# Optimization experiments

Hardware: AMD Instinct MI355X
Metric: run time of the kernel (lower is better)

Reference implementation:

```python
import jax, jax.numpy as jnp
import numpy as np

E, D, H, K, N = 8, 512, 2048, 2, 1024  # experts, d_model, d_hidden, top_k, tokens
EPS = 1e-5


def _moe_linear(x, idx, W, b):
    # x: (M, in); idx: (M,) expert id per row; W: (E, out, in); b: (E, out)
    # Brute-force: compute per-expert dense GEMMs, select via one-hot (matches
    # BruteForceMoELinear math: y[i] = x[i] @ W[idx[i]].T + b[idx[i]]).
    m = jax.nn.one_hot(idx, W.shape[0], dtype=x.dtype)  # (M, E)
    y = jnp.einsum('me,eoi,mi->mo', m, W, x)
    return y + jnp.take(b, idx, axis=0)


def _forward(inp, gate_w, gate_b, w1, b1, w2, b2, ln_w, ln_b):
    # NaiveGate: linear -> top_k -> softmax over top-k logits
    logits = inp @ gate_w.T + gate_b              # (N, E)
    top_val, top_idx = jax.lax.top_k(logits, K)   # (N, K)
    score = jax.nn.softmax(top_val, axis=-1)      # (N, K)
    # repeat_interleave tokens, dispatch to experts
    x = jnp.repeat(inp, K, axis=0)                # (N*K, D)
    idx = top_idx.reshape(-1)                     # (N*K,)
    x = _moe_linear(x, idx, w1, b1)               # (N*K, H)
    x = jax.nn.gelu(x, approximate=False)         # torch F.gelu default = erf
    x = _moe_linear(x, idx, w2, b2)               # (N*K, D)
    x = x.reshape(N, K, D)
    x = jnp.einsum('nk,nkd->nd', score, x)        # bmm((N,1,K),(N,K,D)) combine
    # post layer norm (pre_lnorm=False)
    mu = jnp.mean(x, axis=-1, keepdims=True)
    var = jnp.var(x, axis=-1, keepdims=True)
    return (x - mu) * jax.lax.rsqrt(var + EPS) * ln_w + ln_b


def setup_inputs() -> dict:
    key = jax.random.key(0)
    ks = jax.random.split(key, 8)
    s = 0.02
    return {
        'inp': jax.random.normal(ks[0], (N, D), dtype=jnp.float32),
        'gate_w': s * jax.random.normal(ks[1], (E, D), dtype=jnp.float32),
        'gate_b': jnp.zeros((E,), dtype=jnp.float32),
        'w1': s * jax.random.normal(ks[2], (E, H, D), dtype=jnp.float32),
        'b1': jnp.zeros((E, H), dtype=jnp.float32),
        'w2': s * jax.random.normal(ks[3], (E, D, H), dtype=jnp.float32),
        'b2': jnp.zeros((E, D), dtype=jnp.float32),
        'ln_w': jnp.ones((D,), dtype=jnp.float32),
        'ln_b': jnp.zeros((D,), dtype=jnp.float32),
    }


def reference(inp, gate_w, gate_b, w1, b1, w2, b2, ln_w, ln_b):
    return _forward(inp, gate_w, gate_b, w1, b1, w2, b2, ln_w, ln_b)
```

## Files before the change

### kernel.cpp

```cpp
#include <hip/hip_runtime.h>
#include <cstdint>
#include <cstddef>

typedef _Float16 half_t;
typedef _Float16 half8 __attribute__((ext_vector_type(8)));
typedef float floatx4 __attribute__((ext_vector_type(4)));

#define E_ 8
#define D_ 512
#define H_ 2048
#define NTOK 1024
#define NP 2048
#define TM 64
#define MAX_TILES 40

__device__ __forceinline__ float gelu_f(float x) {
    return 0.5f * x * (1.0f + erff(x * 0.7071067811865476f));
}

__device__ __forceinline__ half8 cvt8(floatx4 a, floatx4 b) {
    half8 h = { (half_t)a[0], (half_t)a[1], (half_t)a[2], (half_t)a[3],
                (half_t)b[0], (half_t)b[1], (half_t)b[2], (half_t)b[3] };
    return h;
}

__global__ __launch_bounds__(256) void gate_kernel(
        const float* __restrict__ inp, const float* __restrict__ gate_w,
        const float* __restrict__ gate_b, float* __restrict__ logits) {
    int n = blockIdx.x * 4 + (threadIdx.x >> 6);
    int lane = threadIdx.x & 63;
    const floatx4* xr = (const floatx4*)(inp + (size_t)n * D_);
    floatx4 x0 = xr[lane * 2], x1 = xr[lane * 2 + 1];
    #pragma unroll
    for (int e = 0; e < E_; e++) {
        const floatx4* gr = (const floatx4*)(gate_w + (size_t)e * D_);
        floatx4 g0 = gr[lane * 2], g1 = gr[lane * 2 + 1];
        float p = x0[0]*g0[0] + x0[1]*g0[1] + x0[2]*g0[2] + x0[3]*g0[3]
                + x1[0]*g1[0] + x1[1]*g1[1] + x1[2]*g1[2] + x1[3]*g1[3];
        #pragma unroll
        for (int m = 1; m < 64; m <<= 1) p += __shfl_xor(p, m);
        if (lane == 0) logits[(size_t)n * E_ + e] = p + gate_b[e];
    }
}

__global__ __launch_bounds__(256) void plan_kernel(
        const float* __restrict__ logits, float* __restrict__ score,
        int* __restrict__ idx, int* __restrict__ pos_of_pair,
        int* __restrict__ tok_of_pos,
        int* __restrict__ tile_e, int* __restrict__ tile_row0,
        int* __restrict__ tile_cnt, int* __restrict__ ntiles) {
    __shared__ int cnt_s[E_], off_s[E_ + 1], cur_s[E_];
    int tid = threadIdx.x;
    if (tid < E_) { cnt_s[tid] = 0; cur_s[tid] = 0; }
    __syncthreads();
    int my_e[4][2];
    #pragma unroll
    for (int i = 0; i < 4; i++) {
        int n = tid + i * 256;
        float l[E_];
        #pragma unroll
        for (int e = 0; e < E_; e++) l[e] = logits[(size_t)n * E_ + e];
        int e0 = 0; float v0 = l[0];
        #pragma unroll
        for (int e = 1; e < E_; e++) if (l[e] > v0) { v0 = l[e]; e0 = e; }
        int e1 = -1; float v1 = -3.4e38f;
        #pragma unroll
        for (int e = 0; e < E_; e++) if (e != e0 && l[e] > v1) { v1 = l[e]; e1 = e; }
        float s1 = expf(v1 - v0);
        float den = 1.0f + s1;
        score[2 * n]     = 1.0f / den;
        score[2 * n + 1] = s1 / den;
        idx[2 * n]     = e0;
        idx[2 * n + 1] = e1;
        atomicAdd(&cnt_s[e0], 1);
        atomicAdd(&cnt_s[e1], 1);
        my_e[i][0] = e0; my_e[i][1] = e1;
    }
    __syncthreads();
    if (tid == 0) {
        int o = 0;
        #pragma unroll
        for (int e = 0; e < E_; e++) { off_s[e] = o; o += cnt_s[e]; }
        off_s[E_] = o;
        int t = 0;
        for (int e = 0; e < E_; e++) {
            int c = cnt_s[e];
            int nt = (c + TM - 1) / TM;
            for (int i = 0; i < nt; i++) {
                tile_e[t] = e;
                tile_row0[t] = off_s[e] + i * TM;
                int rem = c - i * TM;
                tile_cnt[t] = rem < TM ? rem : TM;
                t++;
            }
        }
        ntiles[0] = t;
    }
    __syncthreads();
    #pragma unroll
    for (int i = 0; i < 4; i++) {
        #pragma unroll
        for (int k = 0; k < 2; k++) {
            int p = (tid + i * 256) * 2 + k;
            int e = my_e[i][k];
            int r = atomicAdd(&cur_s[e], 1);
            int pos = off_s[e] + r;
            pos_of_pair[p] = pos;
            tok_of_pos[pos] = p >> 1;
        }
    }
}

__global__ __launch_bounds__(256) void gemm1_kernel(
        const float* __restrict__ inp, const int* __restrict__ tok_of_pos,
        const float* __restrict__ w1, const float* __restrict__ b1,
        const int* __restrict__ tile_e, const int* __restrict__ tile_row0,
        const int* __restrict__ tile_cnt, const int* __restrict__ ntiles,
        half_t* __restrict__ Y1) {
    __shared__ half_t As[2][64 * 64];
    __shared__ half_t Bs[2][64 * 64];
    int flat = blockIdx.x + gridDim.x * blockIdx.y;
    int per = (gridDim.x * gridDim.y) >> 3;
    int f2 = (flat & 7) * per + (flat >> 3);
    int t = f2 % MAX_TILES;
    int cb = f2 / MAX_TILES;
    if (t >= ntiles[0]) return;
    int e = tile_e[t], row0 = tile_row0[t], cnt = tile_cnt[t];
    int colbase = cb * 64;
    int tid = threadIdx.x;
    int wave = tid >> 6, lane = tid & 63;
    int quad = lane >> 4, l16 = lane & 15;
    int wm = (wave & 1) * 32, wn = (wave >> 1) * 32;
    int xm = l16 & 7;

    int gr0 = tid >> 3, gr1 = gr0 + 32, gc = tid & 7;
    int sw0 = gc ^ (gr0 & 7), sw1 = gc ^ (gr1 & 7);
    int ar0 = row0 + gr0; if (ar0 > NP - 1) ar0 = NP - 1;
    int ar1 = row0 + gr1; if (ar1 > NP - 1) ar1 = NP - 1;
    int tok0 = tok_of_pos[ar0];
    int tok1 = tok_of_pos[ar1];
    const floatx4* Ag0 = (const floatx4*)(inp + (size_t)tok0 * D_) + gc * 2;
    const floatx4* Ag1 = (const floatx4*)(inp + (size_t)tok1 * D_) + gc * 2;
    const floatx4* Bg0 = (const floatx4*)(w1 + ((size_t)e * H_ + colbase + gr0) * D_) + gc * 2;
    const floatx4* Bg1 = (const floatx4*)(w1 + ((size_t)e * H_ + colbase + gr1) * D_) + gc * 2;
    int sa0 = gr0 * 64 + sw0 * 8, sa1 = gr1 * 64 + sw1 * 8;

    floatx4 ra0a, ra0b, ra1a, ra1b, rb0a, rb0b, rb1a, rb1b;
    #define LOAD1(kq) do { \
        ra0a = Ag0[kq]; ra0b = Ag0[(kq) + 1]; \
        ra1a = Ag1[kq]; ra1b = Ag1[(kq) + 1]; \
        rb0a = Bg0[kq]; rb0b = Bg0[(kq) + 1]; \
        rb1a = Bg1[kq]; rb1b = Bg1[(kq) + 1]; } while (0)
    #define CVW1(buf) do { \
        *(half8*)(&As[buf][sa0]) = cvt8(ra0a, ra0b); \
        *(half8*)(&As[buf][sa1]) = cvt8(ra1a, ra1b); \
        *(half8*)(&Bs[buf][sa0]) = cvt8(rb0a, rb0b); \
        *(half8*)(&Bs[buf][sa1]) = cvt8(rb1a, rb1b); } while (0)

    floatx4 acc[2][2] = {};
    LOAD1(0);
    CVW1(0);
    __syncthreads();
    int cur = 0;
    for (int k0 = 0; k0 < D_; k0 += 64) {
        bool more = (k0 + 64) < D_;
        if (more) LOAD1((k0 + 64) >> 2);
        const half_t* Ab = &As[cur][0];
        const half_t* Bb = &Bs[cur][0];
        #pragma unroll
        for (int ks = 0; ks < 2; ks++) {
            half8 a[2], b[2];
            #pragma unroll
            for (int mi = 0; mi < 2; mi++)
                a[mi] = *(const half8*)(Ab + (wm + mi * 16 + l16) * 64 + ((ks * 4 + quad) ^ xm) * 8);
            #pragma unroll
            for (int ni = 0; ni < 2; ni++)
                b[ni] = *(const half8*)(Bb + (wn + ni * 16 + l16) * 64 + ((ks * 4 + quad) ^ xm) * 8);
            #pragma unroll
            for (int mi = 0; mi < 2; mi++)
                #pragma unroll
                for (int ni = 0; ni < 2; ni++)
                    acc[mi][ni] = __builtin_amdgcn_mfma_f32_16x16x32_f16(a[mi], b[ni], acc[mi][ni], 0, 0, 0);
        }
        if (more) CVW1(cur ^ 1);
        __syncthreads();
        cur ^= 1;
    }
    #undef LOAD1
    #undef CVW1

    float bias[2];
    #pragma unroll
    for (int ni = 0; ni < 2; ni++)
        bias[ni] = b1[(size_t)e * H_ + colbase + wn + ni * 16 + l16];
    #pragma unroll
    for (int mi = 0; mi < 2; mi++) {
        #pragma unroll
        for (int r = 0; r < 4; r++) {
            int rr = wm + mi * 16 + quad * 4 + r;
            if (rr >= cnt) continue;
            size_t rowoff = (size_t)(row0 + rr) * H_;
            #pragma unroll
            for (int ni = 0; ni < 2; ni++) {
                float v = acc[mi][ni][r] + bias[ni];
                Y1[rowoff + colbase + wn + ni * 16 + l16] = (half_t)gelu_f(v);
            }
        }
    }
}

__global__ __launch_bounds__(256) void gemm2_kernel(
        const half_t* __restrict__ Y1, const float* __restrict__ w2,
        const int* __restrict__ tile_e, const int* __restrict__ tile_row0,
        const int* __restrict__ tile_cnt, const int* __restrict__ ntiles,
        float* __restrict__ Y2p) {
    __shared__ half_t As[2][64 * 64];
    __shared__ half_t Bs[2][64 * 64];
    int flat = blockIdx.x + gridDim.x * (blockIdx.y + gridDim.y * blockIdx.z);
    int per = (gridDim.x * gridDim.y * gridDim.z) >> 3;
    int f2 = (flat & 7) * per + (flat >> 3);
    int t = f2 % MAX_TILES;
    int rest = f2 / MAX_TILES;
    int cb = rest & 7;
    int kz = rest >> 3;
    if (t >= ntiles[0]) return;
    int e = tile_e[t], row0 = tile_row0[t], cnt = tile_cnt[t];
    int colbase = cb * 64;
    int kzbase = kz * 512;
    int tid = threadIdx.x;
    int wave = tid >> 6, lane = tid & 63;
    int quad = lane >> 4, l16 = lane & 15;
    int wm = (wave & 1) * 32, wn = (wave >> 1) * 32;
    int xm = l16 & 7;

    int gr0 = tid >> 3, gr1 = gr0 + 32, gc = tid & 7;
    int sw0 = gc ^ (gr0 & 7), sw1 = gc ^ (gr1 & 7);
    const half8* Ag0 = (const half8*)(Y1 + (size_t)(row0 + gr0) * H_ + kzbase) + gc;
    const half8* Ag1 = (const half8*)(Y1 + (size_t)(row0 + gr1) * H_ + kzbase) + gc;
    const floatx4* Bg0 = (const floatx4*)(w2 + ((size_t)e * D_ + colbase + gr0) * H_ + kzbase) + gc * 2;
    const floatx4* Bg1 = (const floatx4*)(w2 + ((size_t)e * D_ + colbase + gr1) * H_ + kzbase) + gc * 2;
    int sa0 = gr0 * 64 + sw0 * 8, sa1 = gr1 * 64 + sw1 * 8;

    half8 ha0, ha1;
    floatx4 rb0a, rb0b, rb1a, rb1b;
    #define LOAD2(k0) do { \
        ha0 = Ag0[(k0) >> 3]; ha1 = Ag1[(k0) >> 3]; \
        rb0a = Bg0[(k0) >> 2]; rb0b = Bg0[((k0) >> 2) + 1]; \
        rb1a = Bg1[(k0) >> 2]; rb1b = Bg1[((k0) >> 2) + 1]; } while (0)
    #define CVW2(buf) do { \
        *(half8*)(&As[buf][sa0]) = ha0; \
        *(half8*)(&As[buf][sa1]) = ha1; \
        *(half8*)(&Bs[buf][sa0]) = cvt8(rb0a, rb0b); \
        *(half8*)(&Bs[buf][sa1]) = cvt8(rb1a, rb1b); } while (0)

    floatx4 acc[2][2] = {};
    LOAD2(0);
    CVW2(0);
    __syncthreads();
    int cur = 0;
    for (int k0 = 0; k0 < 512; k0 += 64) {
        bool more = (k0 + 64) < 512;
        if (more) LOAD2(k0 + 64);
        const half_t* Ab = &As[cur][0];
        const half_t* Bb = &Bs[cur][0];
        #pragma unroll
        for (int ks = 0; ks < 2; ks++) {
            half8 a[2], b[2];
            #pragma unroll
            for (int mi = 0; mi < 2; mi++)
                a[mi] = *(const half8*)(Ab + (wm + mi * 16 + l16) * 64 + ((ks * 4 + quad) ^ xm) * 8);
            #pragma unroll
            for (int ni = 0; ni < 2; ni++)
                b[ni] = *(const half8*)(Bb + (wn + ni * 16 + l16) * 64 + ((ks * 4 + quad) ^ xm) * 8);
            #pragma unroll
            for (int mi = 0; mi < 2; mi++)
                #pragma unroll
                for (int ni = 0; ni < 2; ni++)
                    acc[mi][ni] = __builtin_amdgcn_mfma_f32_16x16x32_f16(a[mi], b[ni], acc[mi][ni], 0, 0, 0);
        }
        if (more) CVW2(cur ^ 1);
        __syncthreads();
        cur ^= 1;
    }
    #undef LOAD2
    #undef CVW2

    #pragma unroll
    for (int mi = 0; mi < 2; mi++) {
        #pragma unroll
        for (int r = 0; r < 4; r++) {
            int rr = wm + mi * 16 + quad * 4 + r;
            if (rr >= cnt) continue;
            size_t rowoff = ((size_t)kz * NP + row0 + rr) * D_;
            #pragma unroll
            for (int ni = 0; ni < 2; ni++)
                Y2p[rowoff + colbase + wn + ni * 16 + l16] = acc[mi][ni][r];
        }
    }
}

__global__ __launch_bounds__(256) void final_kernel(
        const float* __restrict__ Y2p, const float* __restrict__ b2,
        const int* __restrict__ idx, const float* __restrict__ score,
        const int* __restrict__ pos_of_pair,
        const float* __restrict__ ln_w, const float* __restrict__ ln_b,
        float* __restrict__ out) {
    int n = blockIdx.x * 4 + (threadIdx.x >> 6);
    int lane = threadIdx.x & 63;
    int p0 = pos_of_pair[2 * n], p1 = pos_of_pair[2 * n + 1];
    int e0 = idx[2 * n], e1 = idx[2 * n + 1];
    float s0 = score[2 * n], s1 = score[2 * n + 1];

    const floatx4* b2r0 = (const floatx4*)(b2 + (size_t)e0 * D_);
    const floatx4* b2r1 = (const floatx4*)(b2 + (size_t)e1 * D_);
    floatx4 a_lo = b2r0[lane * 2], a_hi = b2r0[lane * 2 + 1];
    floatx4 c_lo = b2r1[lane * 2], c_hi = b2r1[lane * 2 + 1];
    #pragma unroll
    for (int kz = 0; kz < 4; kz++) {
        const floatx4* r0 = (const floatx4*)(Y2p + ((size_t)kz * NP + p0) * D_);
        const floatx4* r1 = (const floatx4*)(Y2p + ((size_t)kz * NP + p1) * D_);
        a_lo += r0[lane * 2]; a_hi += r0[lane * 2 + 1];
        c_lo += r1[lane * 2]; c_hi += r1[lane * 2 + 1];
    }
    floatx4 y_lo = s0 * a_lo + s1 * c_lo;
    floatx4 y_hi = s0 * a_hi + s1 * c_hi;

    float s = 0.0f, q = 0.0f;
    #pragma unroll
    for (int j = 0; j < 4; j++) {
        s += y_lo[j] + y_hi[j];
        q += y_lo[j] * y_lo[j] + y_hi[j] * y_hi[j];
    }
    #pragma unroll
    for (int m = 1; m < 64; m <<= 1) {
        s += __shfl_xor(s, m);
        q += __shfl_xor(q, m);
    }
    float mean = s * (1.0f / 512.0f);
    float var = q * (1.0f / 512.0f) - mean * mean;
    float inv = 1.0f / sqrtf(var + 1e-5f);

    const floatx4* wv = (const floatx4*)ln_w;
    const floatx4* bv = (const floatx4*)ln_b;
    floatx4 o_lo = (y_lo - mean) * inv * wv[lane * 2]     + bv[lane * 2];
    floatx4 o_hi = (y_hi - mean) * inv * wv[lane * 2 + 1] + bv[lane * 2 + 1];
    floatx4* op = (floatx4*)(out + (size_t)n * D_);
    op[lane * 2] = o_lo;
    op[lane * 2 + 1] = o_hi;
}

extern "C" void kernel_launch(void* const* d_in, const int* in_sizes, int n_in,
                              void* d_out, int out_size, void* d_ws, size_t ws_size,
                              hipStream_t stream) {
    const float* inp    = (const float*)d_in[0];
    const float* gate_w = (const float*)d_in[1];
    const float* gate_b = (const float*)d_in[2];
    const float* w1     = (const float*)d_in[3];
    const float* b1     = (const float*)d_in[4];
    const float* w2     = (const float*)d_in[5];
    const float* b2     = (const float*)d_in[6];
    const float* ln_w   = (const float*)d_in[7];
    const float* ln_b   = (const float*)d_in[8];
    float* out = (float*)d_out;

    char* ws = (char*)d_ws;
    size_t o = 0;
    auto carve = [&](size_t bytes) -> char* {
        char* p = ws + o;
        o += (bytes + 255) & ~(size_t)255;
        return p;
    };
    half_t* Y1  = (half_t*)carve(sizeof(half_t) * (size_t)(NP + 128) * H_);
    float*  Y2p = (float*)carve(sizeof(float) * 4 * (size_t)NP * D_);
    float*  logits = (float*)carve(sizeof(float) * NTOK * E_);
    float*  score  = (float*)carve(sizeof(float) * NP);
    int* idx         = (int*)carve(sizeof(int) * NP);
    int* pos_of_pair = (int*)carve(sizeof(int) * NP);
    int* tok_of_pos  = (int*)carve(sizeof(int) * NP);
    int* tile_e      = (int*)carve(sizeof(int) * MAX_TILES);
    int* tile_row0   = (int*)carve(sizeof(int) * MAX_TILES);
    int* tile_cnt    = (int*)carve(sizeof(int) * MAX_TILES);
    int* ntiles      = (int*)carve(sizeof(int) * 1);

    gate_kernel<<<NTOK / 4, 256, 0, stream>>>(inp, gate_w, gate_b, logits);
    plan_kernel<<<1, 256, 0, stream>>>(logits, score, idx, pos_of_pair, tok_of_pos,
                                       tile_e, tile_row0, tile_cnt, ntiles);
    gemm1_kernel<<<dim3(MAX_TILES, H_ / 64), 256, 0, stream>>>(
        inp, tok_of_pos, w1, b1, tile_e, tile_row0, tile_cnt, ntiles, Y1);
    gemm2_kernel<<<dim3(MAX_TILES, D_ / 64, 4), 256, 0, stream>>>(
        Y1, w2, tile_e, tile_row0, tile_cnt, ntiles, Y2p);
    final_kernel<<<NTOK / 4, 256, 0, stream>>>(Y2p, b2, idx, score, pos_of_pair, ln_w, ln_b, out);
}
```

Measured before the change: 169.5 us.

## Preload full-K weight panel into LDS and remap blocks to XCDs

Both expert GEMM kernels now load the whole 64x512 weight panel (converted to fp16, swizzled) into shared memory once up front, and only the activation tile is double-buffered through the K loop. Block indexing is flattened and remapped so that column blocks, or output columns in gemm2, are tied to the XCD index, which is meant to improve L2 reuse of weights across tiles on the same die. This removes the per-iteration weight load and convert from the main loop. In exchange, shared memory use grows to about 80KB per block, which lowers occupancy, and the up-front weight load is not overlapped with compute.

```diff
diff --git a/kernel.cpp b/kernel.cpp
--- a/kernel.cpp
+++ b/kernel.cpp
@@ -101,12 +101,12 @@
     for (int i = 0; i < 4; i++) {
         #pragma unroll
         for (int k = 0; k < 2; k++) {
-            int p = (tid + i * 256) * 2 + k;
+            int pp = (tid + i * 256) * 2 + k;
             int e = my_e[i][k];
             int r = atomicAdd(&cur_s[e], 1);
             int pos = off_s[e] + r;
-            pos_of_pair[p] = pos;
-            tok_of_pos[pos] = p >> 1;
+            pos_of_pair[pp] = pos;
+            tok_of_pos[pos] = pp >> 1;
         }
     }
 }
@@ -117,56 +117,66 @@
         const int* __restrict__ tile_e, const int* __restrict__ tile_row0,
         const int* __restrict__ tile_cnt, const int* __restrict__ ntiles,
         half_t* __restrict__ Y1) {
+    __shared__ half_t Bs[64 * 512];
     __shared__ half_t As[2][64 * 64];
-    __shared__ half_t Bs[2][64 * 64];
-    int flat = blockIdx.x + gridDim.x * blockIdx.y;
-    int per = (gridDim.x * gridDim.y) >> 3;
-    int f2 = (flat & 7) * per + (flat >> 3);
-    int t = f2 % MAX_TILES;
-    int cb = f2 / MAX_TILES;
+    const int bid = blockIdx.x, tid = threadIdx.x;
+    const int xcd = bid & 7, ib = bid >> 3;
+    const int t = ib % MAX_TILES;
+    const int cb = xcd * 4 + ib / MAX_TILES;
     if (t >= ntiles[0]) return;
-    int e = tile_e[t], row0 = tile_row0[t], cnt = tile_cnt[t];
-    int colbase = cb * 64;
-    int tid = threadIdx.x;
-    int wave = tid >> 6, lane = tid & 63;
-    int quad = lane >> 4, l16 = lane & 15;
-    int wm = (wave & 1) * 32, wn = (wave >> 1) * 32;
-    int xm = l16 & 7;
-
-    int gr0 = tid >> 3, gr1 = gr0 + 32, gc = tid & 7;
-    int sw0 = gc ^ (gr0 & 7), sw1 = gc ^ (gr1 & 7);
+    const int e = tile_e[t], row0 = tile_row0[t], cnt = tile_cnt[t];
+    const int colbase = cb * 64;
+    const int wave = tid >> 6, lane = tid & 63;
+    const int quad = lane >> 4, l16 = lane & 15;
+    const int wm = (wave & 1) * 32, wn = (wave >> 1) * 32;
+    const int xm = l16 & 7;
+
+    const int gr0 = tid >> 3, gr1 = gr0 + 32, gc = tid & 7;
+    const int sw0 = gc ^ (gr0 & 7), sw1 = gc ^ (gr1 & 7);
+    const int sa0 = gr0 * 64 + sw0 * 8, sa1 = gr1 * 64 + sw1 * 8;
     int ar0 = row0 + gr0; if (ar0 > NP - 1) ar0 = NP - 1;
     int ar1 = row0 + gr1; if (ar1 > NP - 1) ar1 = NP - 1;
-    int tok0 = tok_of_pos[ar0];
-    int tok1 = tok_of_pos[ar1];
-    const floatx4* Ag0 = (const floatx4*)(inp + (size_t)tok0 * D_) + gc * 2;
-    const floatx4* Ag1 = (const floatx4*)(inp + (size_t)tok1 * D_) + gc * 2;
-    const floatx4* Bg0 = (const floatx4*)(w1 + ((size_t)e * H_ + colbase + gr0) * D_) + gc * 2;
-    const floatx4* Bg1 = (const floatx4*)(w1 + ((size_t)e * H_ + colbase + gr1) * D_) + gc * 2;
-    int sa0 = gr0 * 64 + sw0 * 8, sa1 = gr1 * 64 + sw1 * 8;
-
-    floatx4 ra0a, ra0b, ra1a, ra1b, rb0a, rb0b, rb1a, rb1b;
-    #define LOAD1(kq) do { \
+    const floatx4* Ag0 = (const floatx4*)(inp + (size_t)tok_of_pos[ar0] * D_) + gc * 2;
+    const floatx4* Ag1 = (const floatx4*)(inp + (size_t)tok_of_pos[ar1] * D_) + gc * 2;
+
+    floatx4 ra0a, ra0b, ra1a, ra1b;
+    #define LOADA(kq) do { \
         ra0a = Ag0[kq]; ra0b = Ag0[(kq) + 1]; \
-        ra1a = Ag1[kq]; ra1b = Ag1[(kq) + 1]; \
-        rb0a = Bg0[kq]; rb0b = Bg0[(kq) + 1]; \
-        rb1a = Bg1[kq]; rb1b = Bg1[(kq) + 1]; } while (0)
-    #define CVW1(buf) do { \
+        ra1a = Ag1[kq]; ra1b = Ag1[(kq) + 1]; } while (0)
+    #define CVWA(buf) do { \
         *(half8*)(&As[buf][sa0]) = cvt8(ra0a, ra0b); \
-        *(half8*)(&As[buf][sa1]) = cvt8(ra1a, ra1b); \
-        *(half8*)(&Bs[buf][sa0]) = cvt8(rb0a, rb0b); \
-        *(half8*)(&Bs[buf][sa1]) = cvt8(rb1a, rb1b); } while (0)
+        *(half8*)(&As[buf][sa1]) = cvt8(ra1a, ra1b); } while (0)
+
+    LOADA(0);
+
+    #pragma unroll
+    for (int hb = 0; hb < 2; hb++) {
+        floatx4 v0[8], v1[8];
+        #pragma unroll
+        for (int u = 0; u < 8; u++) {
+            int gid = tid + (hb * 8 + u) * 256;
+            int row = gid >> 6, g = gid & 63;
+            const floatx4* src = (const floatx4*)(w1 + ((size_t)e * H_ + colbase + row) * D_ + g * 8);
+            v0[u] = src[0]; v1[u] = src[1];
+        }
+        #pragma unroll
+        for (int u = 0; u < 8; u++) {
+            int gid = tid + (hb * 8 + u) * 256;
+            int row = gid >> 6, g = gid & 63;
+            int gs = (g & 56) | ((g ^ row) & 7);
+            *(half8*)(&Bs[row * 512 + gs * 8]) = cvt8(v0[u], v1[u]);
+        }
+    }
+    CVWA(0);
+    __syncthreads();
 
     floatx4 acc[2][2] = {};
-    LOAD1(0);
-    CVW1(0);
-    __syncthreads();
     int cur = 0;
     for (int k0 = 0; k0 < D_; k0 += 64) {
         bool more = (k0 + 64) < D_;
-        if (more) LOAD1((k0 + 64) >> 2);
+        if (more) LOADA((k0 + 64) >> 2);
         const half_t* Ab = &As[cur][0];
-        const half_t* Bb = &Bs[cur][0];
+        const int kg0 = k0 >> 3;
         #pragma unroll
         for (int ks = 0; ks < 2; ks++) {
             half8 a[2], b[2];
@@ -175,19 +185,19 @@
                 a[mi] = *(const half8*)(Ab + (wm + mi * 16 + l16) * 64 + ((ks * 4 + quad) ^ xm) * 8);
             #pragma unroll
             for (int ni = 0; ni < 2; ni++)
-                b[ni] = *(const half8*)(Bb + (wn + ni * 16 + l16) * 64 + ((ks * 4 + quad) ^ xm) * 8);
+                b[ni] = *(const half8*)(&Bs[(wn + ni * 16 + l16) * 512 + (kg0 + ((ks * 4 + quad) ^ xm)) * 8]);
             #pragma unroll
             for (int mi = 0; mi < 2; mi++)
                 #pragma unroll
                 for (int ni = 0; ni < 2; ni++)
                     acc[mi][ni] = __builtin_amdgcn_mfma_f32_16x16x32_f16(a[mi], b[ni], acc[mi][ni], 0, 0, 0);
         }
-        if (more) CVW1(cur ^ 1);
+        if (more) CVWA(cur ^ 1);
         __syncthreads();
         cur ^= 1;
     }
-    #undef LOAD1
-    #undef CVW1
+    #undef LOADA
+    #undef CVWA
 
     float bias[2];
     #pragma unroll
@@ -214,55 +224,64 @@
         const int* __restrict__ tile_e, const int* __restrict__ tile_row0,
         const int* __restrict__ tile_cnt, const int* __restrict__ ntiles,
         float* __restrict__ Y2p) {
+    __shared__ half_t Bs[64 * 512];
     __shared__ half_t As[2][64 * 64];
-    __shared__ half_t Bs[2][64 * 64];
-    int flat = blockIdx.x + gridDim.x * (blockIdx.y + gridDim.y * blockIdx.z);
-    int per = (gridDim.x * gridDim.y * gridDim.z) >> 3;
-    int f2 = (flat & 7) * per + (flat >> 3);
-    int t = f2 % MAX_TILES;
-    int rest = f2 / MAX_TILES;
-    int cb = rest & 7;
-    int kz = rest >> 3;
+    const int bid = blockIdx.x, tid = threadIdx.x;
+    const int xcd = bid & 7, ib = bid >> 3;
+    const int t = ib % MAX_TILES;
+    const int kz = ib / MAX_TILES;
     if (t >= ntiles[0]) return;
-    int e = tile_e[t], row0 = tile_row0[t], cnt = tile_cnt[t];
-    int colbase = cb * 64;
-    int kzbase = kz * 512;
-    int tid = threadIdx.x;
-    int wave = tid >> 6, lane = tid & 63;
-    int quad = lane >> 4, l16 = lane & 15;
-    int wm = (wave & 1) * 32, wn = (wave >> 1) * 32;
-    int xm = l16 & 7;
-
-    int gr0 = tid >> 3, gr1 = gr0 + 32, gc = tid & 7;
-    int sw0 = gc ^ (gr0 & 7), sw1 = gc ^ (gr1 & 7);
+    const int e = tile_e[t], row0 = tile_row0[t], cnt = tile_cnt[t];
+    const int colbase = xcd * 64;
+    const int kzbase = kz * 512;
+    const int wave = tid >> 6, lane = tid & 63;
+    const int quad = lane >> 4, l16 = lane & 15;
+    const int wm = (wave & 1) * 32, wn = (wave >> 1) * 32;
+    const int xm = l16 & 7;
+
+    const int gr0 = tid >> 3, gr1 = gr0 + 32, gc = tid & 7;
+    const int sw0 = gc ^ (gr0 & 7), sw1 = gc ^ (gr1 & 7);
+    const int sa0 = gr0 * 64 + sw0 * 8, sa1 = gr1 * 64 + sw1 * 8;
     const half8* Ag0 = (const half8*)(Y1 + (size_t)(row0 + gr0) * H_ + kzbase) + gc;
     const half8* Ag1 = (const half8*)(Y1 + (size_t)(row0 + gr1) * H_ + kzbase) + gc;
-    const floatx4* Bg0 = (const floatx4*)(w2 + ((size_t)e * D_ + colbase + gr0) * H_ + kzbase) + gc * 2;
-    const floatx4* Bg1 = (const floatx4*)(w2 + ((size_t)e * D_ + colbase + gr1) * H_ + kzbase) + gc * 2;
-    int sa0 = gr0 * 64 + sw0 * 8, sa1 = gr1 * 64 + sw1 * 8;
 
     half8 ha0, ha1;
-    floatx4 rb0a, rb0b, rb1a, rb1b;
-    #define LOAD2(k0) do { \
-        ha0 = Ag0[(k0) >> 3]; ha1 = Ag1[(k0) >> 3]; \
-        rb0a = Bg0[(k0) >> 2]; rb0b = Bg0[((k0) >> 2) + 1]; \
-        rb1a = Bg1[(k0) >> 2]; rb1b = Bg1[((k0) >> 2) + 1]; } while (0)
-    #define CVW2(buf) do { \
+    #define LOADA2(k0) do { \
+        ha0 = Ag0[(k0) >> 3]; ha1 = Ag1[(k0) >> 3]; } while (0)
+    #define CVWA2(buf) do { \
         *(half8*)(&As[buf][sa0]) = ha0; \
-        *(half8*)(&As[buf][sa1]) = ha1; \
-        *(half8*)(&Bs[buf][sa0]) = cvt8(rb0a, rb0b); \
-        *(half8*)(&Bs[buf][sa1]) = cvt8(rb1a, rb1b); } while (0)
+        *(half8*)(&As[buf][sa1]) = ha1; } while (0)
+
+    LOADA2(0);
+
+    #pragma unroll
+    for (int hb = 0; hb < 2; hb++) {
+        floatx4 v0[8], v1[8];
+        #pragma unroll
+        for (int u = 0; u < 8; u++) {
+            int gid = tid + (hb * 8 + u) * 256;
+            int row = gid >> 6, g = gid & 63;
+            const floatx4* src = (const floatx4*)(w2 + ((size_t)e * D_ + colbase + row) * H_ + kzbase + g * 8);
+            v0[u] = src[0]; v1[u] = src[1];
+        }
+        #pragma unroll
+        for (int u = 0; u < 8; u++) {
+            int gid = tid + (hb * 8 + u) * 256;
+            int row = gid >> 6, g = gid & 63;
+            int gs = (g & 56) | ((g ^ row) & 7);
+            *(half8*)(&Bs[row * 512 + gs * 8]) = cvt8(v0[u], v1[u]);
+        }
+    }
+    CVWA2(0);
+    __syncthreads();
 
     floatx4 acc[2][2] = {};
-    LOAD2(0);
-    CVW2(0);
-    __syncthreads();
     int cur = 0;
     for (int k0 = 0; k0 < 512; k0 += 64) {
         bool more = (k0 + 64) < 512;
-        if (more) LOAD2(k0 + 64);
+        if (more) LOADA2(k0 + 64);
         const half_t* Ab = &As[cur][0];
-        const half_t* Bb = &Bs[cur][0];
+        const int kg0 = k0 >> 3;
         #pragma unroll
         for (int ks = 0; ks < 2; ks++) {
             half8 a[2], b[2];
@@ -271,19 +290,19 @@
                 a[mi] = *(const half8*)(Ab + (wm + mi * 16 + l16) * 64 + ((ks * 4 + quad) ^ xm) * 8);
             #pragma unroll
             for (int ni = 0; ni < 2; ni++)
-                b[ni] = *(const half8*)(Bb + (wn + ni * 16 + l16) * 64 + ((ks * 4 + quad) ^ xm) * 8);
+                b[ni] = *(const half8*)(&Bs[(wn + ni * 16 + l16) * 512 + (kg0 + ((ks * 4 + quad) ^ xm)) * 8]);
             #pragma unroll
             for (int mi = 0; mi < 2; mi++)
                 #pragma unroll
                 for (int ni = 0; ni < 2; ni++)
                     acc[mi][ni] = __builtin_amdgcn_mfma_f32_16x16x32_f16(a[mi], b[ni], acc[mi][ni], 0, 0, 0);
         }
-        if (more) CVW2(cur ^ 1);
+        if (more) CVWA2(cur ^ 1);
         __syncthreads();
         cur ^= 1;
     }
-    #undef LOAD2
-    #undef CVW2
+    #undef LOADA2
+    #undef CVWA2
 
     #pragma unroll
     for (int mi = 0; mi < 2; mi++) {
@@ -385,9 +404,9 @@
     gate_kernel<<<NTOK / 4, 256, 0, stream>>>(inp, gate_w, gate_b, logits);
     plan_kernel<<<1, 256, 0, stream>>>(logits, score, idx, pos_of_pair, tok_of_pos,
                                        tile_e, tile_row0, tile_cnt, ntiles);
-    gemm1_kernel<<<dim3(MAX_TILES, H_ / 64), 256, 0, stream>>>(
+    gemm1_kernel<<<MAX_TILES * 32, 256, 0, stream>>>(
         inp, tok_of_pos, w1, b1, tile_e, tile_row0, tile_cnt, ntiles, Y1);
-    gemm2_kernel<<<dim3(MAX_TILES, D_ / 64, 4), 256, 0, stream>>>(
+    gemm2_kernel<<<MAX_TILES * 32, 256, 0, stream>>>(
         Y1, w2, tile_e, tile_row0, tile_cnt, ntiles, Y2p);
     final_kernel<<<NTOK / 4, 256, 0, stream>>>(Y2p, b2, idx, score, pos_of_pair, ln_w, ln_b, out);
 }
```

Measured after the change: 177.1 us. +4.5%, slower.
